# Kernel tuning notes

Hardware: AMD Instinct MI355X
Metric: run time of the kernel (lower is better)

## Reference

```python
import jax, jax.numpy as jnp
import numpy as np

K = 0.1            # manifold curvature param: points satisfy <x,x>_L = -1/K
H = 8              # num_heads
DH = 64            # head_spatial_dim
SP = 512           # spatial_dim = H*DH
SCALE = 1.0 / np.sqrt(DH)
SQRT_K = np.sqrt(K).astype(np.float32)


def _lorentz_fc(x, W, b):
    # Manifold-constrained FC: linear map to spatial coords, time recomputed
    sp = x @ W + b                                            # [..., out_spatial]
    t = jnp.sqrt(jnp.clip(1.0 / K + jnp.sum(sp * sp, axis=-1, keepdims=True), 1e-9, None))
    return jnp.concatenate([t, sp], axis=-1)


def _logmap0(p):
    # Lorentz log map at origin -> tangent spatial coords (time comp = 0)
    t, sp = p[..., :1], p[..., 1:]
    nrm = jnp.sqrt(jnp.sum(sp * sp, axis=-1, keepdims=True))
    theta = jnp.arccosh(jnp.clip(SQRT_K * t, 1.0 + 1e-7, None))
    return (theta / SQRT_K) * sp / jnp.maximum(nrm, 1e-9)


def _expmap0(u):
    nrm = jnp.sqrt(jnp.sum(u * u, axis=-1, keepdims=True))
    t = jnp.cosh(SQRT_K * nrm) / SQRT_K
    sp = jnp.sinh(SQRT_K * nrm) * u / (SQRT_K * jnp.maximum(nrm, 1e-9))
    return jnp.concatenate([t, sp], axis=-1)


def setup_inputs() -> dict:
    key = jax.random.key(0)
    ks = jax.random.split(key, 9)
    B, N = 4, 2048
    space = jax.random.normal(ks[0], (B, N, SP), dtype=jnp.float32) * 0.5
    t = jnp.sqrt(1.0 / K + jnp.sum(space * space, axis=-1, keepdims=True))
    x = jnp.concatenate([t, space], axis=-1)                  # on-manifold [B,N,513]
    s = (1 + SP) ** -0.5
    Wq = jax.random.normal(ks[1], (1 + SP, SP), dtype=jnp.float32) * s
    Wk = jax.random.normal(ks[2], (1 + SP, SP), dtype=jnp.float32) * s
    Wv = jax.random.normal(ks[3], (1 + SP, SP), dtype=jnp.float32) * s
    Wo = jax.random.normal(ks[4], (1 + SP, SP), dtype=jnp.float32) * s
    bq = jax.random.normal(ks[5], (SP,), dtype=jnp.float32) * 0.01
    bk = jax.random.normal(ks[6], (SP,), dtype=jnp.float32) * 0.01
    bv = jax.random.normal(ks[7], (SP,), dtype=jnp.float32) * 0.01
    bo = jax.random.normal(ks[8], (SP,), dtype=jnp.float32) * 0.01
    return {"x": x, "Wq": Wq, "bq": bq, "Wk": Wk, "bk": bk, "Wv": Wv, "bv": bv, "Wo": Wo, "bo": bo}


def _split_heads(p):
    # [B,N,1+H*DH] -> [B,H,N,1+DH], sharing the time component across heads
    B, N, _ = p.shape
    t = p[..., :1]                                            # [B,N,1]
    sp = p[..., 1:].reshape(B, N, H, DH)
    t = jnp.broadcast_to(t[:, :, None, :], (B, N, H, 1))
    return jnp.concatenate([t, sp], axis=-1).transpose(0, 2, 1, 3)


def reference(x, Wq, bq, Wk, bk, Wv, bv, Wo, bo):
    q = _split_heads(_lorentz_fc(x, Wq, bq))                  # [B,H,N,1+DH]
    k = _split_heads(_lorentz_fc(x, Wk, bk))
    v = _split_heads(_lorentz_fc(x, Wv, bv))
    # Lorentzian inner product scores: -q_t k_t + <q_s, k_s>
    scores = (jnp.einsum('bhnd,bhmd->bhnm', q[..., 1:], k[..., 1:])
              - jnp.einsum('bhni,bhmi->bhnm', q[..., :1], k[..., :1])) * SCALE
    attn = jax.nn.softmax(scores, axis=-1)                    # [B,H,N,N]
    # Riemannian aggregation: logmap0 -> weighted sum in tangent space -> expmap0
    v_tan = _logmap0(v)                                       # [B,H,N,DH]
    out_tan = jnp.einsum('bhnm,bhmd->bhnd', attn, v_tan)
    out = _expmap0(out_tan)                                   # [B,H,N,1+DH]
    # direct head concat: stack spatial parts, renormalize time onto manifold
    B, _, N, _ = out.shape
    space_cat = out[..., 1:].transpose(0, 2, 1, 3).reshape(B, N, H * DH)
    t_prime = jnp.sqrt(jnp.clip(1.0 / K + jnp.sum(space_cat * space_cat, axis=-1, keepdims=True), 1e-9, None))
    cat = jnp.concatenate([t_prime, space_cat], axis=-1)      # [B,N,513]
    return _lorentz_fc(cat, Wo, bo)                           # [B,N,513]
```

## Files before the change

### kernel.cpp

```cpp
#include <hip/hip_runtime.h>
#include <math.h>

#define H_    8
#define DH_   64
#define SPD   512
#define NSEQ  2048
#define BATCH 4
#define ROWS  8192
#define KDIM  513
#define KPAD  544
#define INVK  10.0f
#define SQRTK 0.31622776601683794f
#define S2C   0.18033688011112043f
#define LOG2E 1.4426950408889634f
#define TKOFF 12.0f

using bf16x8 = __attribute__((ext_vector_type(8))) short;
using f32x4  = __attribute__((ext_vector_type(4))) float;
using f32x16 = __attribute__((ext_vector_type(16))) float;

static __device__ __forceinline__ short f2bf(float f){
  union { float f; unsigned u; } v; v.f = f;
  unsigned r = v.u + 0x7fffu + ((v.u >> 16) & 1u);
  return (short)(r >> 16);
}
static __device__ __forceinline__ float bf2f(short s){
  union { unsigned u; float f; } v; v.u = ((unsigned)(unsigned short)s) << 16;
  return v.f;
}
static __device__ __forceinline__ unsigned cvtpk(float lo, float hi){
  unsigned r; asm("v_cvt_pk_bf16_f32 %0, %1, %2" : "=v"(r) : "v"(lo), "v"(hi)); return r;
}
static __device__ __forceinline__ void plswapf(float& a, float& b){
  asm("v_permlane32_swap_b32 %0, %1" : "+v"(a), "+v"(b));
}
static __device__ __forceinline__ void plswapu(unsigned& a, unsigned& b){
  asm("v_permlane32_swap_b32 %0, %1" : "+v"(a), "+v"(b));
}
static __device__ __forceinline__ float exp2v(float x){
  float r; asm("v_exp_f32 %0, %1" : "=v"(r) : "v"(x)); return r;
}

__global__ __launch_bounds__(256) void convx_kernel(const float* __restrict__ x,
                                                    short* __restrict__ xb){
  int i = blockIdx.x * 256 + threadIdx.x;
  if (i >= ROWS * KPAD) return;
  int r = i / KPAD, c = i - r * KPAD;
  xb[i] = (c < KDIM) ? f2bf(x[(size_t)r * KDIM + c]) : (short)0;
}

__global__ __launch_bounds__(256) void convw_kernel(const float* __restrict__ Wq,
                                                    const float* __restrict__ Wk,
                                                    const float* __restrict__ Wv,
                                                    const float* __restrict__ Wo,
                                                    short* __restrict__ WT){
  int wsel = blockIdx.y;
  const float* W = (wsel == 0) ? Wq : (wsel == 1) ? Wk : (wsel == 2) ? Wv : Wo;
  int i = blockIdx.x * 256 + threadIdx.x;
  if (i >= SPD * KPAD) return;
  int n = i / KPAD, k = i - n * KPAD;
  WT[(size_t)wsel * SPD * KPAD + i] = (k < KDIM) ? f2bf(W[(size_t)k * SPD + n]) : (short)0;
}

template<bool BF16OUT>
__global__ __launch_bounds__(256) void gemm_kernel(
    const short* __restrict__ A, const short* __restrict__ WTbase,
    int sel0, int sel1, int sel2,
    const float* __restrict__ bias0, const float* __restrict__ bias1,
    const float* __restrict__ bias2,
    void* __restrict__ C0, void* __restrict__ C1, void* __restrict__ C2,
    int ldc, int coff)
{
  const int z = blockIdx.z;
  const int sel = (z == 0) ? sel0 : (z == 1) ? sel1 : sel2;
  const short* BT = WTbase + (size_t)sel * SPD * KPAD;
  const float* bias = (z == 0) ? bias0 : (z == 1) ? bias1 : bias2;
  void* C = (z == 0) ? C0 : (z == 1) ? C1 : C2;

  __shared__ short As[128 * 32];
  __shared__ short Bs[128 * 32];

  const int tid  = threadIdx.x;
  const int lane = tid & 63;
  const int wave = tid >> 6;
  const int row0 = blockIdx.x * 128;
  const int col0 = blockIdx.y * 128;
  const int wr = (wave >> 1) * 64;
  const int wc = (wave & 1) * 64;
  const int rA  = lane & 15;
  const int kg2 = (lane >> 4) * 16;

  f32x4 acc[4][4] = {};

  for (int kt = 0; kt < KPAD / 32; ++kt){
    __syncthreads();
    #pragma unroll
    for (int p = 0; p < 2; ++p){
      const int idx = p * 256 + tid;
      const int r = idx >> 2;
      const int cb = (idx & 3) * 8;
      const uint4 va = *(const uint4*)(A  + (size_t)(row0 + r) * KPAD + kt * 32 + cb);
      const uint4 vb = *(const uint4*)(BT + (size_t)(col0 + r) * KPAD + kt * 32 + cb);
      const int off = (r * 64 + cb * 2) ^ ((r & 3) << 4);
      *(uint4*)((char*)As + off) = va;
      *(uint4*)((char*)Bs + off) = vb;
    }
    __syncthreads();
    bf16x8 af[4], bfr[4];
    #pragma unroll
    for (int m = 0; m < 4; ++m){
      const int r = wr + m * 16 + rA;
      af[m] = *(const bf16x8*)((const char*)As + ((r * 64 + kg2) ^ ((r & 3) << 4)));
    }
    #pragma unroll
    for (int n = 0; n < 4; ++n){
      const int r = wc + n * 16 + rA;
      bfr[n] = *(const bf16x8*)((const char*)Bs + ((r * 64 + kg2) ^ ((r & 3) << 4)));
    }
    #pragma unroll
    for (int m = 0; m < 4; ++m)
      #pragma unroll
      for (int n = 0; n < 4; ++n)
        acc[m][n] = __builtin_amdgcn_mfma_f32_16x16x32_bf16(af[m], bfr[n], acc[m][n], 0, 0, 0);
  }

  #pragma unroll
  for (int m = 0; m < 4; ++m){
    const int row = row0 + wr + m * 16 + (lane >> 4) * 4;
    #pragma unroll
    for (int n = 0; n < 4; ++n){
      const int col = col0 + wc + n * 16 + rA;
      const float bv = bias[col];
      #pragma unroll
      for (int j = 0; j < 4; ++j){
        const float v = acc[m][n][j] + bv;
        if (BF16OUT) ((short*)C)[(size_t)(row + j) * SPD + col] = f2bf(v);
        else         ((float*)C)[(size_t)(row + j) * ldc + coff + col] = v;
      }
    }
  }
}

__global__ __launch_bounds__(512) void postqkv_kernel(
    const short* __restrict__ qb, const short* __restrict__ kb,
    const short* __restrict__ vb, float* __restrict__ tq,
    unsigned* __restrict__ tkpk, short* __restrict__ vtT)
{
  const int row = blockIdx.x;
  const int t = threadIdx.x;
  const int lane = t & 63;
  const int w = t >> 6;
  __shared__ float red[8];

  float q = bf2f(qb[(size_t)row * SPD + t]);
  float s = q * q;
  #pragma unroll
  for (int m = 32; m; m >>= 1) s += __shfl_xor(s, m, 64);
  if (lane == 0) red[w] = s;
  __syncthreads();
  float tot = 0.f;
  #pragma unroll
  for (int i = 0; i < 8; ++i) tot += red[i];
  if (t == 0) tq[row] = sqrtf(INVK + tot);
  __syncthreads();

  float kk = bf2f(kb[(size_t)row * SPD + t]);
  s = kk * kk;
  #pragma unroll
  for (int m = 32; m; m >>= 1) s += __shfl_xor(s, m, 64);
  if (lane == 0) red[w] = s;
  __syncthreads();
  tot = 0.f;
  #pragma unroll
  for (int i = 0; i < 8; ++i) tot += red[i];
  if (t == 0){
    const float tkv = sqrtf(INVK + tot);
    const float tkm = tkv - TKOFF;
    const short bhi = f2bf(tkm);
    const short blo = f2bf(tkm - bf2f(bhi));
    tkpk[row] = (unsigned)(unsigned short)bhi | ((unsigned)(unsigned short)blo << 16);
  }
  __syncthreads();

  float v = bf2f(vb[(size_t)row * SPD + t]);
  s = v * v;
  #pragma unroll
  for (int m = 32; m; m >>= 1) s += __shfl_xor(s, m, 64);
  if (lane == 0) red[w] = s;
  __syncthreads();
  tot = 0.f;
  #pragma unroll
  for (int i = 0; i < 8; ++i) tot += red[i];
  const float tv = sqrtf(INVK + tot);
  const float av = fmaxf(SQRTK * tv, 1.0f + 1e-7f);
  const float theta = __logf(av + sqrtf(av * av - 1.0f));
  const float fac = theta * (1.0f / SQRTK);
  const float nrm = sqrtf(s);
  const float vt = fac * v / fmaxf(nrm, 1e-9f);
  const int b = row >> 11, n = row & (NSEQ - 1);
  vtT[((size_t)((b * H_ + w) * DH_ + lane)) * NSEQ + n] = f2bf(vt);
}

__global__ __launch_bounds__(256) void attn_kernel(
    const short* __restrict__ qb, const short* __restrict__ kb,
    const short* __restrict__ vtT, const float* __restrict__ tqg,
    const unsigned* __restrict__ tkpk, short* __restrict__ catb)
{
  int bid = blockIdx.x;
  bid = (bid & 7) * 64 + (bid >> 3);
  const int qt = bid & 15;
  const int bh = bid >> 4;
  const int b = bh >> 3, h = bh & 7;
  const int q0 = qt * 128;
  const int tid = threadIdx.x;
  const int lane = tid & 63;
  const int w = tid >> 6;
  const int l31 = lane & 31;
  const int hi = lane >> 5;
  const int rsw = (l31 & 7) << 4;

  __shared__ short Ks[2][64 * 64];
  __shared__ short Vs[2][64 * 64];
  __shared__ float lred[4][32];
  __shared__ unsigned tks[NSEQ];

  const int qrow = q0 + w * 32 + l31;
  bf16x8 qf[4];
  {
    const short* qptr = qb + (size_t)(b * NSEQ + qrow) * SPD + h * DH_ + hi * 8;
    #pragma unroll
    for (int s = 0; s < 4; ++s){
      union { bf16x8 v; short e[8]; } u;
      u.v = *(const bf16x8*)(qptr + s * 16);
      #pragma unroll
      for (int j = 0; j < 8; ++j) u.e[j] = f2bf(bf2f(u.e[j]) * S2C);
      qf[s] = u.v;
    }
  }
  bf16x8 qf4;
  {
    const float a = -S2C * tqg[b * NSEQ + qrow];
    const short ahi = f2bf(a);
    const short alo = f2bf(a - bf2f(ahi));
    union { unsigned u[4]; bf16x8 v; } q4;
    q4.u[0] = hi ? 0u : ((unsigned)(unsigned short)ahi | ((unsigned)(unsigned short)alo << 16));
    q4.u[1] = hi ? 0u : (unsigned)(unsigned short)ahi;
    q4.u[2] = 0; q4.u[3] = 0;
    qf4 = q4.v;
  }

  {
    const unsigned* tsrc = tkpk + b * NSEQ + tid * 8;
    *(uint4*)&tks[tid * 8]     = *(const uint4*)tsrc;
    *(uint4*)&tks[tid * 8 + 4] = *(const uint4*)(tsrc + 4);
  }

  const int rB = tid >> 3;
  const int c0 = (tid & 7) * 16;
  const int cc = c0 ^ ((rB & 7) << 4);
  const short* kbase = kb + (size_t)(b * NSEQ) * SPD + h * DH_;
  const short* vbase = vtT + (size_t)(bh * DH_) * NSEQ;

  uint4 kA0, kA1, vA0, vA1;
  uint4 kB0, kB1, vB0, vB1;

#define LOADA(m0) do{ \
    kA0 = *(const uint4*)(kbase + (size_t)((m0) + rB) * SPD + (c0 >> 1)); \
    kA1 = *(const uint4*)(kbase + (size_t)((m0) + 32 + rB) * SPD + (c0 >> 1)); \
    vA0 = *(const uint4*)(vbase + (size_t)rB * NSEQ + (m0) + (c0 >> 1)); \
    vA1 = *(const uint4*)(vbase + (size_t)(32 + rB) * NSEQ + (m0) + (c0 >> 1)); }while(0)
#define LOADB(m0) do{ \
    kB0 = *(const uint4*)(kbase + (size_t)((m0) + rB) * SPD + (c0 >> 1)); \
    kB1 = *(const uint4*)(kbase + (size_t)((m0) + 32 + rB) * SPD + (c0 >> 1)); \
    vB0 = *(const uint4*)(vbase + (size_t)rB * NSEQ + (m0) + (c0 >> 1)); \
    vB1 = *(const uint4*)(vbase + (size_t)(32 + rB) * NSEQ + (m0) + (c0 >> 1)); }while(0)
#define WRITEA(buf) do{ \
    *(uint4*)((char*)Ks[buf] + rB * 128 + cc) = kA0; \
    *(uint4*)((char*)Ks[buf] + (32 + rB) * 128 + cc) = kA1; \
    *(uint4*)((char*)Vs[buf] + rB * 128 + cc) = vA0; \
    *(uint4*)((char*)Vs[buf] + (32 + rB) * 128 + cc) = vA1; }while(0)
#define WRITEB(buf) do{ \
    *(uint4*)((char*)Ks[buf] + rB * 128 + cc) = kB0; \
    *(uint4*)((char*)Ks[buf] + (32 + rB) * 128 + cc) = kB1; \
    *(uint4*)((char*)Vs[buf] + rB * 128 + cc) = vB0; \
    *(uint4*)((char*)Vs[buf] + (32 + rB) * 128 + cc) = vB1; }while(0)
#define BARRIER() asm volatile("s_waitcnt lgkmcnt(0)\n\ts_barrier" ::: "memory")
#define WAITV4()  asm volatile("s_waitcnt vmcnt(4)" ::: "memory")
#define WAITV0()  asm volatile("s_waitcnt vmcnt(0)" ::: "memory")

  float l_run = 0.f;
  f32x16 o[2] = {};

  auto KAUG = [&](unsigned pk)->bf16x8{
    union { unsigned u[4]; bf16x8 v; } ka;
    ka.u[0] = hi ? 0u : ((pk & 0xFFFFu) | (pk << 16));
    ka.u[1] = hi ? 0u : (pk >> 16);
    ka.u[2] = 0; ka.u[3] = 0;
    return ka.v;
  };

  auto COMPUTE = [&](const char* Kc, const char* Vc, int m0){
    const unsigned pk0 = tks[m0 + l31];
    const unsigned pk1 = tks[m0 + 32 + l31];

    f32x16 sacc[2] = {};
    __builtin_amdgcn_s_setprio(1);
    #pragma unroll
    for (int f = 0; f < 2; ++f){
      const int rowb = (f * 32 + l31) * 128;
      #pragma unroll
      for (int s = 0; s < 4; ++s){
        const bf16x8 kf = *(const bf16x8*)(Kc + rowb + ((s * 32 + hi * 16) ^ rsw));
        sacc[f] = __builtin_amdgcn_mfma_f32_32x32x16_bf16(kf, qf[s], sacc[f], 0, 0, 0);
      }
    }
    sacc[0] = __builtin_amdgcn_mfma_f32_32x32x16_bf16(KAUG(pk0), qf4, sacc[0], 0, 0, 0);
    sacc[1] = __builtin_amdgcn_mfma_f32_32x32x16_bf16(KAUG(pk1), qf4, sacc[1], 0, 0, 0);
    __builtin_amdgcn_s_setprio(0);

    #pragma unroll
    for (int f = 0; f < 2; ++f)
      #pragma unroll
      for (int e = 0; e < 16; ++e)
        sacc[f][e] = exp2v(sacc[f][e]);

    float s16[16];
    #pragma unroll
    for (int e = 0; e < 16; ++e) s16[e] = sacc[0][e] + sacc[1][e];
    #pragma unroll
    for (int st = 8; st; st >>= 1)
      #pragma unroll
      for (int e = 0; e < st; ++e) s16[e] += s16[e + st];
    float rs = s16[0];
    { float ca = rs, cb = rs; plswapf(ca, cb); rs += hi ? ca : cb; }
    l_run += rs;

    bf16x8 pa[4];
    #pragma unroll
    for (int f = 0; f < 2; ++f)
      #pragma unroll
      for (int g16 = 0; g16 < 2; ++g16){
        const int bse = g16 * 8;
        unsigned A0 = cvtpk(sacc[f][bse + 0], sacc[f][bse + 1]);
        unsigned A1 = cvtpk(sacc[f][bse + 2], sacc[f][bse + 3]);
        unsigned B0 = cvtpk(sacc[f][bse + 4], sacc[f][bse + 5]);
        unsigned B1 = cvtpk(sacc[f][bse + 6], sacc[f][bse + 7]);
        plswapu(A0, B0);
        plswapu(A1, B1);
        union { unsigned u[4]; bf16x8 v; } pu;
        pu.u[0] = A0; pu.u[1] = A1; pu.u[2] = B0; pu.u[3] = B1;
        pa[f * 2 + g16] = pu.v;
      }

    __builtin_amdgcn_s_setprio(1);
    #pragma unroll
    for (int db = 0; db < 2; ++db){
      const int rowb = (db * 32 + l31) * 128;
      #pragma unroll
      for (int ks = 0; ks < 4; ++ks){
        const bf16x8 vf = *(const bf16x8*)(Vc + rowb + ((ks * 32 + hi * 16) ^ rsw));
        o[db] = __builtin_amdgcn_mfma_f32_32x32x16_bf16(pa[ks], vf, o[db], 0, 0, 0);
      }
    }
    __builtin_amdgcn_s_setprio(0);
  };

  LOADA(0);
  WAITV0();
  WRITEA(0);
  __syncthreads();
  LOADB(64);

  const int NT = NSEQ / 64;
  #pragma unroll 1
  for (int t = 0; t < NT; t += 2){
    const int m0 = t * 64;
    if (t + 2 < NT) LOADA(m0 + 128);
    COMPUTE((const char*)Ks[0], (const char*)Vs[0], m0);
    if (t + 2 < NT) WAITV4(); else WAITV0();
    WRITEB(1);
    BARRIER();
    if (t + 3 < NT) LOADB(m0 + 192);
    COMPUTE((const char*)Ks[1], (const char*)Vs[1], m0 + 64);
    if (t + 2 < NT){
      if (t + 3 < NT) WAITV4(); else WAITV0();
      WRITEA(0);
    }
    BARRIER();
  }

  if (lane < 32) lred[w][l31] = l_run;
  asm volatile("s_waitcnt lgkmcnt(0)" ::: "memory");
  f32x4 lv[4];
  #pragma unroll
  for (int g = 0; g < 4; ++g) lv[g] = *(const f32x4*)&lred[w][8 * g + 4 * hi];

  const size_t obase = (size_t)(b * NSEQ + q0 + w * 32) * KPAD + 1 + h * DH_ + l31;
  #pragma unroll
  for (int e = 0; e < 16; ++e){
    const float linv = __builtin_amdgcn_rcpf(lv[e >> 2][e & 3]);
    const float ov0 = o[0][e] * linv;
    const float ov1 = o[1][e] * linv;
    float ss = ov0 * ov0 + ov1 * ov1;
    #pragma unroll
    for (int off = 16; off; off >>= 1) ss += __shfl_xor(ss, off, 64);
    const float nrm = sqrtf(ss);
    const float e2 = exp2f(SQRTK * nrm * LOG2E);
    const float einv = __builtin_amdgcn_rcpf(e2);
    const float fac = (e2 - einv) * 0.5f * __builtin_amdgcn_rcpf(SQRTK * fmaxf(nrm, 1e-9f));
    const int crow = (e & 3) + 8 * (e >> 2) + 4 * hi;
    catb[obase + (size_t)crow * KPAD]      = f2bf(fac * ov0);
    catb[obase + (size_t)crow * KPAD + 32] = f2bf(fac * ov1);
  }
#undef LOADA
#undef LOADB
#undef WRITEA
#undef WRITEB
#undef BARRIER
#undef WAITV4
#undef WAITV0
}

__global__ __launch_bounds__(512) void tprime_kernel(short* __restrict__ catb){
  const int row = blockIdx.x;
  const int t = threadIdx.x, lane = t & 63, w = t >> 6;
  __shared__ float red[8];
  float v = bf2f(catb[(size_t)row * KPAD + 1 + t]);
  float s = v * v;
  #pragma unroll
  for (int m = 32; m; m >>= 1) s += __shfl_xor(s, m, 64);
  if (lane == 0) red[w] = s;
  __syncthreads();
  float tot = 0.f;
  #pragma unroll
  for (int i = 0; i < 8; ++i) tot += red[i];
  if (t == 0) catb[(size_t)row * KPAD] = f2bf(sqrtf(fmaxf(INVK + tot, 1e-9f)));
  if (t < KPAD - KDIM) catb[(size_t)row * KPAD + KDIM + t] = 0;
}

__global__ __launch_bounds__(512) void finalize_kernel(float* __restrict__ out){
  const int row = blockIdx.x;
  const int t = threadIdx.x, lane = t & 63, w = t >> 6;
  __shared__ float red[8];
  float v = out[(size_t)row * KDIM + 1 + t];
  float s = v * v;
  #pragma unroll
  for (int m = 32; m; m >>= 1) s += __shfl_xor(s, m, 64);
  if (lane == 0) red[w] = s;
  __syncthreads();
  float tot = 0.f;
  #pragma unroll
  for (int i = 0; i < 8; ++i) tot += red[i];
  if (t == 0) out[(size_t)row * KDIM] = sqrtf(fmaxf(INVK + tot, 1e-9f));
}

extern "C" void kernel_launch(void* const* d_in, const int* in_sizes, int n_in,
                              void* d_out, int out_size, void* d_ws, size_t ws_size,
                              hipStream_t stream)
{
  (void)in_sizes; (void)n_in; (void)out_size; (void)ws_size;
  const float* x  = (const float*)d_in[0];
  const float* Wq = (const float*)d_in[1];
  const float* bq = (const float*)d_in[2];
  const float* Wk = (const float*)d_in[3];
  const float* bk = (const float*)d_in[4];
  const float* Wv = (const float*)d_in[5];
  const float* bv = (const float*)d_in[6];
  const float* Wo = (const float*)d_in[7];
  const float* bo = (const float*)d_in[8];
  float* out = (float*)d_out;

  char* p = (char*)d_ws;
  short* xb   = (short*)p; p += (size_t)ROWS * KPAD * 2;
  short* WT   = (short*)p; p += (size_t)4 * SPD * KPAD * 2;
  short* qb   = (short*)p; p += (size_t)ROWS * SPD * 2;
  short* kb   = (short*)p; p += (size_t)ROWS * SPD * 2;
  short* vb   = (short*)p; p += (size_t)ROWS * SPD * 2;
  short* vtT  = (short*)p; p += (size_t)ROWS * SPD * 2;
  float* tq   = (float*)p; p += (size_t)ROWS * 4;
  unsigned* tkpk = (unsigned*)p; p += (size_t)ROWS * 4;
  short* catb = (short*)p; p += (size_t)ROWS * KPAD * 2;

  convx_kernel<<<(ROWS * KPAD) / 256, 256, 0, stream>>>(x, xb);
  convw_kernel<<<dim3((SPD * KPAD + 255) / 256, 4), 256, 0, stream>>>(Wq, Wk, Wv, Wo, WT);
  gemm_kernel<true><<<dim3(64, 4, 3), 256, 0, stream>>>(
      xb, WT, 0, 1, 2, bq, bk, bv, qb, kb, vb, SPD, 0);
  postqkv_kernel<<<ROWS, 512, 0, stream>>>(qb, kb, vb, tq, tkpk, vtT);
  attn_kernel<<<512, 256, 0, stream>>>(qb, kb, vtT, tq, tkpk, catb);
  tprime_kernel<<<ROWS, 512, 0, stream>>>(catb);
  gemm_kernel<false><<<dim3(64, 4, 1), 256, 0, stream>>>(
      catb, WT, 3, 3, 3, bo, bo, bo, out, out, out, KDIM, 1);
  finalize_kernel<<<ROWS, 512, 0, stream>>>(out);
}
```

Before: 167.6 us.

## Use direct global-to-LDS loads in GEMM, smaller output tile, wave-per-row postqkv

The GEMM now loads tiles with global_load_lds, going straight from global memory to LDS without a register round trip, and uses a new swizzle that matches the linear LDS destination. The output projection GEMM uses a 64-row tile, doubling the block count so more CUs are busy. postqkv is restructured so each wave handles two rows with 8-element vector loads and pure shuffle reductions, removing the shared-memory reductions and block barriers. The risks are the extra wait on vmcnt(0) each iteration and the scattered 2-byte stores into the transposed vtT buffer.

```diff
diff --git a/kernel.cpp b/kernel.cpp
--- a/kernel.cpp
+++ b/kernel.cpp
@@ -41,6 +41,10 @@
   float r; asm("v_exp_f32 %0, %1" : "=v"(r) : "v"(x)); return r;
 }
 
+#define GL16(gp, lp) __builtin_amdgcn_global_load_lds( \
+    (const __attribute__((address_space(1))) void*)(gp), \
+    (__attribute__((address_space(3))) void*)(lp), 16, 0, 0)
+
 __global__ __launch_bounds__(256) void convx_kernel(const float* __restrict__ x,
                                                     short* __restrict__ xb){
   int i = blockIdx.x * 256 + threadIdx.x;
@@ -62,7 +66,7 @@
   WT[(size_t)wsel * SPD * KPAD + i] = (k < KDIM) ? f2bf(W[(size_t)k * SPD + n]) : (short)0;
 }
 
-template<bool BF16OUT>
+template<bool BF16OUT, int BM>
 __global__ __launch_bounds__(256) void gemm_kernel(
     const short* __restrict__ A, const short* __restrict__ WTbase,
     int sel0, int sel1, int sel2,
@@ -71,56 +75,61 @@
     void* __restrict__ C0, void* __restrict__ C1, void* __restrict__ C2,
     int ldc, int coff)
 {
+  constexpr int NREP = (BM == 128) ? 4 : 2;
   const int z = blockIdx.z;
   const int sel = (z == 0) ? sel0 : (z == 1) ? sel1 : sel2;
   const short* BT = WTbase + (size_t)sel * SPD * KPAD;
   const float* bias = (z == 0) ? bias0 : (z == 1) ? bias1 : bias2;
   void* C = (z == 0) ? C0 : (z == 1) ? C1 : C2;
 
-  __shared__ short As[128 * 32];
+  __shared__ short As[BM * 32];
   __shared__ short Bs[128 * 32];
 
   const int tid  = threadIdx.x;
   const int lane = tid & 63;
   const int wave = tid >> 6;
-  const int row0 = blockIdx.x * 128;
+  const int row0 = blockIdx.x * BM;
   const int col0 = blockIdx.y * 128;
-  const int wr = (wave >> 1) * 64;
-  const int wc = (wave & 1) * 64;
+  const int wr = (BM == 128) ? (wave >> 1) * 64 : 0;
+  const int wc = (BM == 128) ? (wave & 1) * 64 : wave * 32;
   const int rA  = lane & 15;
   const int kg2 = (lane >> 4) * 16;
 
-  f32x4 acc[4][4] = {};
+  f32x4 acc[4][NREP] = {};
 
   for (int kt = 0; kt < KPAD / 32; ++kt){
     __syncthreads();
     #pragma unroll
+    for (int p = 0; p < BM / 64; ++p){
+      const int idx = p * 256 + tid;
+      const int r = idx >> 2, c4 = idx & 3;
+      const int gc = (c4 ^ ((r >> 1) & 3)) * 8;
+      GL16(A + (size_t)(row0 + r) * KPAD + kt * 32 + gc, (char*)As + idx * 16);
+    }
+    #pragma unroll
     for (int p = 0; p < 2; ++p){
       const int idx = p * 256 + tid;
-      const int r = idx >> 2;
-      const int cb = (idx & 3) * 8;
-      const uint4 va = *(const uint4*)(A  + (size_t)(row0 + r) * KPAD + kt * 32 + cb);
-      const uint4 vb = *(const uint4*)(BT + (size_t)(col0 + r) * KPAD + kt * 32 + cb);
-      const int off = (r * 64 + cb * 2) ^ ((r & 3) << 4);
-      *(uint4*)((char*)As + off) = va;
-      *(uint4*)((char*)Bs + off) = vb;
-    }
+      const int r = idx >> 2, c4 = idx & 3;
+      const int gc = (c4 ^ ((r >> 1) & 3)) * 8;
+      GL16(BT + (size_t)(col0 + r) * KPAD + kt * 32 + gc, (char*)Bs + idx * 16);
+    }
+    asm volatile("s_waitcnt vmcnt(0)" ::: "memory");
     __syncthreads();
-    bf16x8 af[4], bfr[4];
+    bf16x8 af[4], bfr[NREP];
     #pragma unroll
     for (int m = 0; m < 4; ++m){
       const int r = wr + m * 16 + rA;
-      af[m] = *(const bf16x8*)((const char*)As + ((r * 64 + kg2) ^ ((r & 3) << 4)));
-    }
-    #pragma unroll
-    for (int n = 0; n < 4; ++n){
+      af[m] = *(const bf16x8*)((const char*)As + ((r * 64 + kg2) ^ (((r >> 1) & 3) << 4)));
+    }
+    #pragma unroll
+    for (int n = 0; n < NREP; ++n){
       const int r = wc + n * 16 + rA;
-      bfr[n] = *(const bf16x8*)((const char*)Bs + ((r * 64 + kg2) ^ ((r & 3) << 4)));
+      bfr[n] = *(const bf16x8*)((const char*)Bs + ((r * 64 + kg2) ^ (((r >> 1) & 3) << 4)));
     }
     #pragma unroll
     for (int m = 0; m < 4; ++m)
       #pragma unroll
-      for (int n = 0; n < 4; ++n)
+      for (int n = 0; n < NREP; ++n)
         acc[m][n] = __builtin_amdgcn_mfma_f32_16x16x32_bf16(af[m], bfr[n], acc[m][n], 0, 0, 0);
   }
 
@@ -128,7 +137,7 @@
   for (int m = 0; m < 4; ++m){
     const int row = row0 + wr + m * 16 + (lane >> 4) * 4;
     #pragma unroll
-    for (int n = 0; n < 4; ++n){
+    for (int n = 0; n < NREP; ++n){
       const int col = col0 + wc + n * 16 + rA;
       const float bv = bias[col];
       #pragma unroll
@@ -141,64 +150,71 @@
   }
 }
 
-__global__ __launch_bounds__(512) void postqkv_kernel(
+__global__ __launch_bounds__(256) void postqkv_kernel(
     const short* __restrict__ qb, const short* __restrict__ kb,
     const short* __restrict__ vb, float* __restrict__ tq,
     unsigned* __restrict__ tkpk, short* __restrict__ vtT)
 {
-  const int row = blockIdx.x;
-  const int t = threadIdx.x;
-  const int lane = t & 63;
-  const int w = t >> 6;
-  __shared__ float red[8];
-
-  float q = bf2f(qb[(size_t)row * SPD + t]);
-  float s = q * q;
-  #pragma unroll
-  for (int m = 32; m; m >>= 1) s += __shfl_xor(s, m, 64);
-  if (lane == 0) red[w] = s;
-  __syncthreads();
-  float tot = 0.f;
-  #pragma unroll
-  for (int i = 0; i < 8; ++i) tot += red[i];
-  if (t == 0) tq[row] = sqrtf(INVK + tot);
-  __syncthreads();
-
-  float kk = bf2f(kb[(size_t)row * SPD + t]);
-  s = kk * kk;
-  #pragma unroll
-  for (int m = 32; m; m >>= 1) s += __shfl_xor(s, m, 64);
-  if (lane == 0) red[w] = s;
-  __syncthreads();
-  tot = 0.f;
-  #pragma unroll
-  for (int i = 0; i < 8; ++i) tot += red[i];
-  if (t == 0){
-    const float tkv = sqrtf(INVK + tot);
-    const float tkm = tkv - TKOFF;
-    const short bhi = f2bf(tkm);
-    const short blo = f2bf(tkm - bf2f(bhi));
-    tkpk[row] = (unsigned)(unsigned short)bhi | ((unsigned)(unsigned short)blo << 16);
-  }
-  __syncthreads();
-
-  float v = bf2f(vb[(size_t)row * SPD + t]);
-  s = v * v;
-  #pragma unroll
-  for (int m = 32; m; m >>= 1) s += __shfl_xor(s, m, 64);
-  if (lane == 0) red[w] = s;
-  __syncthreads();
-  tot = 0.f;
-  #pragma unroll
-  for (int i = 0; i < 8; ++i) tot += red[i];
-  const float tv = sqrtf(INVK + tot);
-  const float av = fmaxf(SQRTK * tv, 1.0f + 1e-7f);
-  const float theta = __logf(av + sqrtf(av * av - 1.0f));
-  const float fac = theta * (1.0f / SQRTK);
-  const float nrm = sqrtf(s);
-  const float vt = fac * v / fmaxf(nrm, 1e-9f);
-  const int b = row >> 11, n = row & (NSEQ - 1);
-  vtT[((size_t)((b * H_ + w) * DH_ + lane)) * NSEQ + n] = f2bf(vt);
+  const int tid = threadIdx.x;
+  const int lane = tid & 63;
+  const int wv = tid >> 6;
+  const int row0 = blockIdx.x * 8 + wv * 2;
+  const int b = blockIdx.x >> 8;
+
+  #pragma unroll
+  for (int i = 0; i < 2; ++i){
+    const int row = row0 + i;
+    const int n = row & (NSEQ - 1);
+    {
+      union { bf16x8 v; short e[8]; } u;
+      u.v = *(const bf16x8*)(qb + (size_t)row * SPD + lane * 8);
+      float s = 0.f;
+      #pragma unroll
+      for (int j = 0; j < 8; ++j){ const float f = bf2f(u.e[j]); s += f * f; }
+      #pragma unroll
+      for (int m = 1; m <= 32; m <<= 1) s += __shfl_xor(s, m, 64);
+      if (lane == 0) tq[row] = sqrtf(INVK + s);
+    }
+    {
+      union { bf16x8 v; short e[8]; } u;
+      u.v = *(const bf16x8*)(kb + (size_t)row * SPD + lane * 8);
+      float s = 0.f;
+      #pragma unroll
+      for (int j = 0; j < 8; ++j){ const float f = bf2f(u.e[j]); s += f * f; }
+      #pragma unroll
+      for (int m = 1; m <= 32; m <<= 1) s += __shfl_xor(s, m, 64);
+      if (lane == 0){
+        const float tkm = sqrtf(INVK + s) - TKOFF;
+        const short bhi = f2bf(tkm);
+        const short blo = f2bf(tkm - bf2f(bhi));
+        tkpk[row] = (unsigned)(unsigned short)bhi | ((unsigned)(unsigned short)blo << 16);
+      }
+    }
+    {
+      union { bf16x8 v; short e[8]; } u;
+      u.v = *(const bf16x8*)(vb + (size_t)row * SPD + lane * 8);
+      float f[8]; float sh = 0.f;
+      #pragma unroll
+      for (int j = 0; j < 8; ++j){ f[j] = bf2f(u.e[j]); sh += f[j] * f[j]; }
+      sh += __shfl_xor(sh, 1, 64);
+      sh += __shfl_xor(sh, 2, 64);
+      sh += __shfl_xor(sh, 4, 64);
+      float tot = sh;
+      tot += __shfl_xor(tot, 8, 64);
+      tot += __shfl_xor(tot, 16, 64);
+      tot += __shfl_xor(tot, 32, 64);
+      const float tv = sqrtf(INVK + tot);
+      const float av = fmaxf(SQRTK * tv, 1.0f + 1e-7f);
+      const float theta = __logf(av + sqrtf(av * av - 1.0f));
+      const float fac = theta * (1.0f / SQRTK);
+      const float inv = fac / fmaxf(sqrtf(sh), 1e-9f);
+      const int h = lane >> 3;
+      const int d0 = (lane & 7) * 8;
+      short* dst = vtT + ((size_t)((b * H_ + h) * DH_ + d0)) * NSEQ + n;
+      #pragma unroll
+      for (int j = 0; j < 8; ++j) dst[(size_t)j * NSEQ] = f2bf(inv * f[j]);
+    }
+  }
 }
 
 __global__ __launch_bounds__(256) void attn_kernel(
@@ -483,12 +499,12 @@
 
   convx_kernel<<<(ROWS * KPAD) / 256, 256, 0, stream>>>(x, xb);
   convw_kernel<<<dim3((SPD * KPAD + 255) / 256, 4), 256, 0, stream>>>(Wq, Wk, Wv, Wo, WT);
-  gemm_kernel<true><<<dim3(64, 4, 3), 256, 0, stream>>>(
+  gemm_kernel<true, 128><<<dim3(64, 4, 3), 256, 0, stream>>>(
       xb, WT, 0, 1, 2, bq, bk, bv, qb, kb, vb, SPD, 0);
-  postqkv_kernel<<<ROWS, 512, 0, stream>>>(qb, kb, vb, tq, tkpk, vtT);
+  postqkv_kernel<<<1024, 256, 0, stream>>>(qb, kb, vb, tq, tkpk, vtT);
   attn_kernel<<<512, 256, 0, stream>>>(qb, kb, vtT, tq, tkpk, catb);
   tprime_kernel<<<ROWS, 512, 0, stream>>>(catb);
-  gemm_kernel<false><<<dim3(64, 4, 1), 256, 0, stream>>>(
+  gemm_kernel<false, 64><<<dim3(128, 4, 1), 256, 0, stream>>>(
       catb, WT, 3, 3, 3, bo, bo, bo, out, out, out, KDIM, 1);
   finalize_kernel<<<ROWS, 512, 0, stream>>>(out);
 }
```

Result: faster. 158.9 us (-5.2%).
